# Kernel optimization log

Hardware: AMD Instinct MI355X
Metric: run time of the kernel (lower is better)

## Reference

```python
import jax, jax.numpy as jnp
import numpy as np

N = 100000   # nodes
E = 400000   # edges per relation
K = 2        # n_hop relations
D = 256      # in_dim
ATT = 64     # att_dim
L = 3        # n_layer
H1, H2 = 128, 64
EPS = 1e-5
NEG_SLOPE = 0.01


def setup_inputs() -> dict:
    key = jax.random.key(0)
    ks = jax.random.split(key, 16)
    s = 1.0 / np.sqrt(D)
    return {
        "x": jax.random.normal(ks[0], (N, D), jnp.float32),
        "edges_index": jax.random.randint(ks[1], (K, 2, E), 0, N),
        "edges_weight": jax.random.uniform(ks[2], (K, E), jnp.float32),
        "bn_gamma": jnp.ones((D,), jnp.float32),
        "bn_beta": jnp.zeros((D,), jnp.float32),
        "gcn_W": jax.random.normal(ks[3], (L, D, D), jnp.float32) * s,
        "gcn_b": jnp.zeros((L, D), jnp.float32),
        "att_lin_W": jax.random.normal(ks[4], (L, K, D, ATT), jnp.float32) * s,
        "att_lin_b": jnp.zeros((L, K, ATT), jnp.float32),
        "att_q": jax.random.normal(ks[5], (L, K, ATT), jnp.float32) * (1.0 / np.sqrt(ATT)),
        "proj_W1": jax.random.normal(ks[6], (D, H1), jnp.float32) * s,
        "proj_b1": jnp.zeros((H1,), jnp.float32),
        "proj_W2": jax.random.normal(ks[7], (H1, H2), jnp.float32) * (1.0 / np.sqrt(H1)),
        "proj_b2": jnp.zeros((H2,), jnp.float32),
    }


def _gcn_aggregate(row, col, w, xw):
    # symmetric gcn_norm on adj_t (add_self_loops=False):
    # deg[i] = sum of w over edges with col == i
    deg = jax.ops.segment_sum(w, col, num_segments=N)
    dinv = jnp.where(deg > 0, 1.0 / jnp.sqrt(deg), 0.0)
    norm = dinv[col] * w * dinv[row]                       # [E]
    # out[c] += norm * xw[r]
    return jax.ops.segment_sum(norm[:, None] * xw[row], col, num_segments=N)


def reference(x, edges_index, edges_weight, bn_gamma, bn_beta, gcn_W, gcn_b,
              att_lin_W, att_lin_b, att_q, proj_W1, proj_b1, proj_W2, proj_b2):
    # BatchNorm1d (training-mode batch stats)
    mu = jnp.mean(x, axis=0)
    var = jnp.mean((x - mu) ** 2, axis=0)
    h = (x - mu) / jnp.sqrt(var + EPS) * bn_gamma + bn_beta   # [N, D]

    rows = edges_index[:, 0, :]  # [K, E]
    cols = edges_index[:, 1, :]

    for i in range(L):
        xw = h @ gcn_W[i]                                     # shared transform [N, D]
        # per-relation sparse aggregation, vmapped over K
        xs = jax.vmap(_gcn_aggregate, in_axes=(0, 0, 0, None))(
            rows, cols, edges_weight, xw) + gcn_b[i]          # [K, N, D]
        # HanAtt: softmax over hops of per-node scores
        keys = jnp.tanh(jnp.einsum('knd,kdh->knh', xs, att_lin_W[i]) + att_lin_b[i][:, None, :])
        sim = jnp.einsum('knh,kh->kn', keys, att_q[i])        # [K, N]
        alpha = jax.nn.softmax(sim, axis=0)                   # softmax over K
        h = jnp.einsum('knd,kn->nd', xs, alpha)               # [N, D]
        h = jax.nn.relu(h)

    h = jax.nn.leaky_relu(h @ proj_W1 + proj_b1, NEG_SLOPE)
    h = jax.nn.leaky_relu(h @ proj_W2 + proj_b2, NEG_SLOPE)
    return h
```

## Files before the change

kernel.cpp:

```cpp
#include <hip/hip_runtime.h>
#include <hip/hip_bf16.h>
#include <math.h>

#define NN 100000
#define EE 400000
#define KD 2
#define DD 256
#define ATTD 64
#define LL 3
#define HH1 128
#define HH2 64
#define EPSV 1e-5f
#define SLOPE 0.01f
#define KN (KD * NN)

typedef short short8 __attribute__((ext_vector_type(8)));
typedef float floatx4 __attribute__((ext_vector_type(4)));
typedef unsigned int u32x4 __attribute__((ext_vector_type(4)));
typedef unsigned short u16;
typedef unsigned int u32;
typedef unsigned long long u64;

__device__ __forceinline__ u16 f2bf(float f) {
    u32 u = __float_as_uint(f);
    return (u16)((u + 0x7fffu + ((u >> 16) & 1u)) >> 16);
}
__device__ __forceinline__ float bf2f(u16 h) {
    return __uint_as_float((u32)h << 16);
}

__global__ void bn_stats(const float* __restrict__ x, float* __restrict__ sums) {
    int d = threadIdx.x;
    int r0 = blockIdx.x * 125;
    float s = 0.f, sq = 0.f;
    for (int r = r0; r < r0 + 125; ++r) {
        float v = x[(size_t)r * DD + d];
        s += v; sq += v * v;
    }
    atomicAdd(&sums[d], s);
    atomicAdd(&sums[DD + d], sq);
}

__global__ void bn_apply(const float* __restrict__ x, const float* __restrict__ sums,
                         const float* __restrict__ gamma, const float* __restrict__ beta,
                         u16* __restrict__ h_hi, u16* __restrict__ h_lo) {
    size_t i = (size_t)blockIdx.x * blockDim.x + threadIdx.x;
    const float inv_n = 1.f / NN;
    int dq = (int)(i & 63) * 4;
    float4 xv = ((const float4*)x)[i];
    ushort4 hv, lv;
    float* xp = (float*)&xv;
    u16* hp = (u16*)&hv; u16* lp = (u16*)&lv;
#pragma unroll
    for (int j = 0; j < 4; ++j) {
        int d = dq + j;
        float mu = sums[d] * inv_n;
        float var = sums[DD + d] * inv_n - mu * mu;
        float inv = rsqrtf(var + EPSV);
        float v = (xp[j] - mu) * inv * gamma[d] + beta[d];
        u16 hb = f2bf(v);
        hp[j] = hb;
        lp[j] = f2bf(v - bf2f(hb));
    }
    ((ushort4*)h_hi)[i] = hv;
    ((ushort4*)h_lo)[i] = lv;
}

__global__ void deg_count(const int* __restrict__ ei, const float* __restrict__ w,
                          float* __restrict__ deg, int* __restrict__ counts) {
    int i = blockIdx.x * blockDim.x + threadIdx.x;
    if (i >= KD * EE) return;
    int k = i / EE, e = i - k * EE;
    int col = ei[(size_t)k * 2 * EE + EE + e];
    atomicAdd(&deg[k * NN + col], w[i]);
    atomicAdd(&counts[k * NN + col], 1);
}

__global__ void dinv_kernel(float* __restrict__ d) {
    int i = blockIdx.x * blockDim.x + threadIdx.x;
    if (i >= KD * NN) return;
    float v = d[i];
    d[i] = v > 0.f ? 1.f / sqrtf(v) : 0.f;
}

#define SCAN_NB ((KN + 255) / 256)
__global__ void scan_blocks(int* __restrict__ starts, int* __restrict__ bsums) {
    __shared__ int tmp[256];
    int t = threadIdx.x;
    int idx = blockIdx.x * 256 + t;
    int v = (idx < KN) ? starts[idx] : 0;
    tmp[t] = v;
    __syncthreads();
#pragma unroll
    for (int off = 1; off < 256; off <<= 1) {
        int s = (t >= off) ? tmp[t - off] : 0;
        __syncthreads();
        tmp[t] += s;
        __syncthreads();
    }
    if (idx < KN) starts[idx] = tmp[t] - v;
    if (t == 255) bsums[blockIdx.x] = tmp[255];
}

__global__ void scan_sums(int* __restrict__ bsums) {
    __shared__ int tmp[1024];
    int t = threadIdx.x;
    int v = (t < SCAN_NB) ? bsums[t] : 0;
    tmp[t] = v;
    __syncthreads();
#pragma unroll
    for (int off = 1; off < 1024; off <<= 1) {
        int s = (t >= off) ? tmp[t - off] : 0;
        __syncthreads();
        tmp[t] += s;
        __syncthreads();
    }
    if (t < SCAN_NB) bsums[t] = tmp[t] - v;
}

__global__ void scan_add(int* __restrict__ starts, const int* __restrict__ bsums) {
    int idx = blockIdx.x * 256 + threadIdx.x;
    if (idx < KN) starts[idx] += bsums[blockIdx.x];
}

__global__ void csr_fill(const int* __restrict__ ei, const float* __restrict__ w,
                         const float* __restrict__ dinv,
                         int* __restrict__ starts, int2* __restrict__ edata) {
    int i = blockIdx.x * blockDim.x + threadIdx.x;
    if (i >= KD * EE) return;
    int k = i / EE, e = i - k * EE;
    const int* eik = ei + (size_t)k * 2 * EE;
    int row = eik[e], col = eik[EE + e];
    float nv = dinv[k * NN + col] * w[i] * dinv[k * NN + row];
    int pos = atomicAdd(&starts[k * NN + col], 1);
    edata[pos] = make_int2(row, __float_as_int(nv));
}

__device__ __forceinline__ void fma_row8(float4& a0, float4& a1, uint4 w, float nv) {
    float2 f0 = __bfloat1622float2(*(const __hip_bfloat162*)&w.x);
    float2 f1 = __bfloat1622float2(*(const __hip_bfloat162*)&w.y);
    float2 f2 = __bfloat1622float2(*(const __hip_bfloat162*)&w.z);
    float2 f3 = __bfloat1622float2(*(const __hip_bfloat162*)&w.w);
    a0.x += nv * f0.x; a0.y += nv * f0.y; a0.z += nv * f1.x; a0.w += nv * f1.y;
    a1.x += nv * f2.x; a1.y += nv * f2.y; a1.z += nv * f3.x; a1.w += nv * f3.y;
}

__global__ __launch_bounds__(256) void gather_agg(
        const int* __restrict__ starts, const int2* __restrict__ edata,
        const u16* __restrict__ xw, u16* __restrict__ xs) {
    int wv = blockIdx.x * 4 + (threadIdx.x >> 6);
    int lane = threadIdx.x & 63;
    int half = lane >> 5, l32 = lane & 31;
    int widx = wv * 2 + half;
    if (widx >= KN) return;
    int begin = widx ? starts[widx - 1] : 0;
    int end = starts[widx];
    int deg = end - begin;
    float4 acc0 = make_float4(0.f, 0.f, 0.f, 0.f);
    float4 acc1 = make_float4(0.f, 0.f, 0.f, 0.f);

    int2 ed = (l32 < deg) ? edata[begin + l32] : make_int2(0, 0);
    int dmain = deg > 32 ? 32 : deg;
    int base = half << 5;

    int j = 0;
    for (; j + 4 <= dmain; j += 4) {
        int r0 = __shfl(ed.x, base + j),     r1 = __shfl(ed.x, base + j + 1);
        int r2 = __shfl(ed.x, base + j + 2), r3 = __shfl(ed.x, base + j + 3);
        float n0 = __int_as_float(__shfl(ed.y, base + j));
        float n1 = __int_as_float(__shfl(ed.y, base + j + 1));
        float n2 = __int_as_float(__shfl(ed.y, base + j + 2));
        float n3 = __int_as_float(__shfl(ed.y, base + j + 3));
        uint4 w0 = *(const uint4*)(xw + (size_t)r0 * DD + l32 * 8);
        uint4 w1 = *(const uint4*)(xw + (size_t)r1 * DD + l32 * 8);
        uint4 w2 = *(const uint4*)(xw + (size_t)r2 * DD + l32 * 8);
        uint4 w3 = *(const uint4*)(xw + (size_t)r3 * DD + l32 * 8);
        fma_row8(acc0, acc1, w0, n0);
        fma_row8(acc0, acc1, w1, n1);
        fma_row8(acc0, acc1, w2, n2);
        fma_row8(acc0, acc1, w3, n3);
    }
    for (; j < dmain; ++j) {
        int r = __shfl(ed.x, base + j);
        float nv = __int_as_float(__shfl(ed.y, base + j));
        uint4 w = *(const uint4*)(xw + (size_t)r * DD + l32 * 8);
        fma_row8(acc0, acc1, w, nv);
    }
    for (int e = begin + 32; e < end; ++e) {
        int2 ee = edata[e];
        float nv = __int_as_float(ee.y);
        uint4 w = *(const uint4*)(xw + (size_t)ee.x * DD + l32 * 8);
        fma_row8(acc0, acc1, w, nv);
    }

    u32x4 st;
    st.x = (u32)f2bf(acc0.x) | ((u32)f2bf(acc0.y) << 16);
    st.y = (u32)f2bf(acc0.z) | ((u32)f2bf(acc0.w) << 16);
    st.z = (u32)f2bf(acc1.x) | ((u32)f2bf(acc1.y) << 16);
    st.w = (u32)f2bf(acc1.z) | ((u32)f2bf(acc1.w) << 16);
    __builtin_nontemporal_store(st, (u32x4*)(xs + (size_t)widx * DD + l32 * 8));
}

#define GCN_T (LL * DD * DD)
#define ATT_T (LL * KD * DD * ATTD)
#define P1_T  (DD * HH1)
#define P2_T  (HH1 * HH2)
#define WC_TOTAL (GCN_T + ATT_T + P1_T + P2_T)
__device__ __forceinline__ void wconv1(const float* __restrict__ W, u16* __restrict__ Wt,
                                       int i, int Kd, int Nc) {
    int kk = i / Nc, n = i - kk * Nc;
    Wt[(size_t)n * Kd + kk] = f2bf(W[i]);
}
__global__ void wconv_all(const float* __restrict__ gcnW, u16* __restrict__ gcnWb,
                          const float* __restrict__ attW, u16* __restrict__ attWb,
                          const float* __restrict__ pW1, u16* __restrict__ pW1b,
                          const float* __restrict__ pW2, u16* __restrict__ pW2b) {
    int gid = blockIdx.x * 256 + threadIdx.x;
    if (gid >= WC_TOTAL) return;
    if (gid < GCN_T) {
        int l = gid >> 16, i = gid & 65535;
        wconv1(gcnW + (size_t)l * DD * DD, gcnWb + (size_t)l * DD * DD, i, DD, DD);
    } else if (gid < GCN_T + ATT_T) {
        int g = gid - GCN_T;
        int lk = g >> 14, i = g & 16383;
        wconv1(attW + (size_t)lk * DD * ATTD, attWb + (size_t)lk * ATTD * DD, i, DD, ATTD);
    } else if (gid < GCN_T + ATT_T + P1_T) {
        wconv1(pW1, pW1b, gid - (GCN_T + ATT_T), DD, HH1);
    } else {
        wconv1(pW2, pW2b, gid - (GCN_T + ATT_T + P1_T), HH1, HH2);
    }
}

__global__ void att_bias_fold(const float* __restrict__ attW, const float* __restrict__ attb,
                              const float* __restrict__ gcnb, float* __restrict__ batt) {
    int lk = blockIdx.x;
    int a = threadIdx.x;
    int l = lk >> 1;
    const float* W = attW + (size_t)lk * DD * ATTD;
    const float* gb = gcnb + l * DD;
    float s = attb[lk * ATTD + a];
    for (int d = 0; d < DD; ++d) s += gb[d] * W[d * ATTD + a];
    batt[lk * ATTD + a] = s;
}

#define LDSP 40

template<int BN_, int MODE, bool PRESPLIT, bool BIAS, int ACT>
__global__ __launch_bounds__(256) void gemm_mfma(
        const float* __restrict__ A,
        const u16* __restrict__ Ahi, const u16* __restrict__ Alo,
        const u16* __restrict__ Bt, const float* __restrict__ bias,
        float* __restrict__ Cf, u16* __restrict__ Cb,
        int M, int Kd, int Nc) {
    constexpr int JW = BN_ / 64;
    __shared__ u16 AsHi[64 * LDSP];
    __shared__ u16 AsLo[64 * LDSP];
    __shared__ u16 Bs[BN_ * LDSP];

    const int tid = threadIdx.x;
    const int lane = tid & 63, wx = tid >> 6;
    const int lane15 = lane & 15, quad = lane >> 4;
    const int bm = blockIdx.x * 64;
    const int bn = blockIdx.y * BN_;

    floatx4 acc[4][JW];
#pragma unroll
    for (int i = 0; i < 4; ++i)
#pragma unroll
        for (int j = 0; j < JW; ++j) acc[i][j] = (floatx4){0.f, 0.f, 0.f, 0.f};

    for (int k0 = 0; k0 < Kd; k0 += 32) {
        if constexpr (PRESPLIT) {
            {
                int m = tid >> 2, ko = (tid & 3) << 3;
                uint4 vh = make_uint4(0, 0, 0, 0), vl = make_uint4(0, 0, 0, 0);
                if (bm + m < M) {
                    vh = *(const uint4*)(Ahi + (size_t)(bm + m) * Kd + k0 + ko);
                    vl = *(const uint4*)(Alo + (size_t)(bm + m) * Kd + k0 + ko);
                }
                *(uint4*)(void*)(AsHi + m * LDSP + ko) = vh;
                *(uint4*)(void*)(AsLo + m * LDSP + ko) = vl;
            }
        } else {
#pragma unroll
            for (int t = tid; t < 512; t += 256) {
                int m = t >> 3, k4 = (t & 7) << 2;
                float4 v = make_float4(0.f, 0.f, 0.f, 0.f);
                if (bm + m < M) v = *(const float4*)(A + (size_t)(bm + m) * Kd + k0 + k4);
                u16 h0 = f2bf(v.x), h1 = f2bf(v.y), h2 = f2bf(v.z), h3 = f2bf(v.w);
                *(ushort4*)(void*)(AsHi + m * LDSP + k4) = make_ushort4(h0, h1, h2, h3);
                u16 l0 = f2bf(v.x - bf2f(h0)), l1 = f2bf(v.y - bf2f(h1));
                u16 l2 = f2bf(v.z - bf2f(h2)), l3 = f2bf(v.w - bf2f(h3));
                *(ushort4*)(void*)(AsLo + m * LDSP + k4) = make_ushort4(l0, l1, l2, l3);
            }
        }
#pragma unroll
        for (int t = tid; t < BN_ * 4; t += 256) {
            int n = t >> 2, ko = (t & 3) << 3;
            uint4 w = *(const uint4*)(Bt + (size_t)(bn + n) * Kd + k0 + ko);
            *(uint4*)(void*)(Bs + n * LDSP + ko) = w;
        }
        __syncthreads();

        const u16* pA  = AsHi + lane15 * LDSP + quad * 8;
        const u16* pAl = AsLo + lane15 * LDSP + quad * 8;
        const u16* pB  = Bs + (wx * (BN_ / 4) + lane15) * LDSP + quad * 8;
        short8 b[JW];
#pragma unroll
        for (int j = 0; j < JW; ++j) b[j] = *(const short8*)(pB + j * 16 * LDSP);
#pragma unroll
        for (int i = 0; i < 4; ++i) {
            short8 a = *(const short8*)(pA + i * 16 * LDSP);
#pragma unroll
            for (int j = 0; j < JW; ++j)
                acc[i][j] = __builtin_amdgcn_mfma_f32_16x16x32_bf16(a, b[j], acc[i][j], 0, 0, 0);
        }
#pragma unroll
        for (int i = 0; i < 4; ++i) {
            short8 a = *(const short8*)(pAl + i * 16 * LDSP);
#pragma unroll
            for (int j = 0; j < JW; ++j)
                acc[i][j] = __builtin_amdgcn_mfma_f32_16x16x32_bf16(a, b[j], acc[i][j], 0, 0, 0);
        }
        __syncthreads();
    }

#pragma unroll
    for (int i = 0; i < 4; ++i) {
#pragma unroll
        for (int r = 0; r < 4; ++r) {
            int row = bm + i * 16 + quad * 4 + r;
            if (row >= M) continue;
#pragma unroll
            for (int j = 0; j < JW; ++j) {
                int col = bn + wx * (BN_ / 4) + j * 16 + lane15;
                float v = acc[i][j][r];
                if constexpr (BIAS) v += bias[col];
                if constexpr (ACT == 1) v = v > 0.f ? v : SLOPE * v;
                if constexpr (MODE == 0) Cf[(size_t)row * Nc + col] = v;
                else                     Cb[(size_t)row * Nc + col] = f2bf(v);
            }
        }
    }
}

__global__ __launch_bounds__(256, 4) void att_combine(
        const u16* __restrict__ xs, const u16* __restrict__ Bt,
        const float* __restrict__ batt, const float* __restrict__ qv,
        const float* __restrict__ gcnb,
        u16* __restrict__ h_hi, u16* __restrict__ h_lo) {
    __shared__ float simbuf[KD][2][64];

    const int tid = threadIdx.x;
    const int lane = tid & 63, waveid = tid >> 6;
    const int kw = waveid >> 1, ch = waveid & 1;
    const int lane15 = lane & 15, quad = lane >> 4;
    const int bm = blockIdx.x * 64;

    short8 bf[8][2];
#pragma unroll
    for (int t = 0; t < 8; ++t)
#pragma unroll
        for (int j = 0; j < 2; ++j) {
            int col = ch * 32 + j * 16 + lane15;
            bf[t][j] = *(const short8*)(Bt + (size_t)kw * ATTD * DD +
                                        (size_t)col * DD + t * 32 + quad * 8);
        }

    floatx4 acc[4][2];
#pragma unroll
    for (int i = 0; i < 4; ++i)
#pragma unroll
        for (int j = 0; j < 2; ++j) acc[i][j] = (floatx4){0.f, 0.f, 0.f, 0.f};

#pragma unroll
    for (int i = 0; i < 4; ++i) {
        int row = bm + i * 16 + lane15;
        row = row < NN ? row : 0;
        const u16* pa = xs + ((size_t)kw * NN + row) * DD + quad * 8;
#pragma unroll
        for (int t = 0; t < 8; ++t) {
            short8 a = *(const short8*)(pa + t * 32);
            acc[i][0] = __builtin_amdgcn_mfma_f32_16x16x32_bf16(a, bf[t][0], acc[i][0], 0, 0, 0);
            acc[i][1] = __builtin_amdgcn_mfma_f32_16x16x32_bf16(a, bf[t][1], acc[i][1], 0, 0, 0);
        }
    }

#pragma unroll
    for (int i = 0; i < 4; ++i) {
#pragma unroll
        for (int r = 0; r < 4; ++r) {
            float p = 0.f;
#pragma unroll
            for (int j = 0; j < 2; ++j) {
                int col = ch * 32 + j * 16 + lane15;
                float v = acc[i][j][r] + batt[kw * ATTD + col];
                float ex = __expf(2.f * v);
                float th = 1.f - 2.f / (ex + 1.f);
                p += th * qv[kw * ATTD + col];
            }
            p += __shfl_xor(p, 1, 64);
            p += __shfl_xor(p, 2, 64);
            p += __shfl_xor(p, 4, 64);
            p += __shfl_xor(p, 8, 64);
            if (lane15 == 0) simbuf[kw][ch][i * 16 + quad * 4 + r] = p;
        }
    }
    __syncthreads();

#pragma unroll 4
    for (int it = 0; it < 8; ++it) {
        int item = tid + it * 256;
        int row = item >> 5, c8 = item & 31;
        int grow = bm + row;
        if (grow >= NN) continue;
        float s0 = simbuf[0][0][row] + simbuf[0][1][row];
        float s1 = simbuf[1][0][row] + simbuf[1][1][row];
        float m = fmaxf(s0, s1);
        float e0 = __expf(s0 - m), e1 = __expf(s1 - m);
        float inv = 1.f / (e0 + e1);
        float a0 = e0 * inv, a1 = e1 * inv;
        uint4 x0 = *(const uint4*)(xs + (size_t)grow * DD + c8 * 8);
        uint4 x1 = *(const uint4*)(xs + ((size_t)NN + grow) * DD + c8 * 8);
        const float* bp = gcnb + c8 * 8;
        uint4 hiw, low;
        u16* hp = (u16*)&hiw; u16* lp = (u16*)&low;
        const u32* xp0 = (const u32*)&x0; const u32* xp1 = (const u32*)&x1;
#pragma unroll
        for (int j = 0; j < 4; ++j) {
            float2 f0 = __bfloat1622float2(*(const __hip_bfloat162*)&xp0[j]);
            float2 f1 = __bfloat1622float2(*(const __hip_bfloat162*)&xp1[j]);
            float ra = fmaxf(0.f, a0 * f0.x + a1 * f1.x + bp[2 * j]);
            float rb = fmaxf(0.f, a0 * f0.y + a1 * f1.y + bp[2 * j + 1]);
            u16 ha = f2bf(ra), hb = f2bf(rb);
            hp[2 * j] = ha; hp[2 * j + 1] = hb;
            lp[2 * j] = f2bf(ra - bf2f(ha));
            lp[2 * j + 1] = f2bf(rb - bf2f(hb));
        }
        *(uint4*)(h_hi + (size_t)grow * DD + c8 * 8) = hiw;
        *(uint4*)(h_lo + (size_t)grow * DD + c8 * 8) = low;
    }
}

extern "C" void kernel_launch(void* const* d_in, const int* in_sizes, int n_in,
                              void* d_out, int out_size, void* d_ws, size_t ws_size,
                              hipStream_t stream) {
    const float* x     = (const float*)d_in[0];
    const int*   ei    = (const int*)d_in[1];
    const float* ew    = (const float*)d_in[2];
    const float* gamma = (const float*)d_in[3];
    const float* beta  = (const float*)d_in[4];
    const float* gcn_W = (const float*)d_in[5];
    const float* gcn_b = (const float*)d_in[6];
    const float* att_W = (const float*)d_in[7];
    const float* att_b = (const float*)d_in[8];
    const float* att_q = (const float*)d_in[9];
    const float* pW1   = (const float*)d_in[10];
    const float* pb1   = (const float*)d_in[11];
    const float* pW2   = (const float*)d_in[12];
    const float* pb2   = (const float*)d_in[13];
    float* out = (float*)d_out;

    char* wsb = (char*)d_ws;
    size_t off = 0;
    auto alloc = [&](size_t bytes) -> void* {
        void* p = wsb + off;
        off += (bytes + 255) & ~(size_t)255;
        return p;
    };
    u16*   xs    = (u16*)alloc((size_t)KD * NN * DD * 2);
    u16*   h_hi  = (u16*)alloc((size_t)NN * DD * 2);
    u16*   h_lo  = (u16*)alloc((size_t)NN * DD * 2);
    u16*   xw    = (u16*)alloc((size_t)NN * DD * 2);
    float* p1tmp = (float*)xw;
    float* dinv  = (float*)alloc((size_t)KN * 4);
    int*   starts= (int*)alloc(((size_t)KN + 1) * 4);
    int2*  edata = (int2*)alloc((size_t)KD * EE * 8);
    float* bnsums= (float*)alloc(2 * DD * 4);
    u16*   gcnWb = (u16*)alloc((size_t)LL * DD * DD * 2);
    u16*   attWb = (u16*)alloc((size_t)LL * KD * ATTD * DD * 2);
    u16*   pW1b  = (u16*)alloc((size_t)HH1 * DD * 2);
    u16*   pW2b  = (u16*)alloc((size_t)HH2 * HH1 * 2);
    float* batt  = (float*)alloc((size_t)LL * KD * ATTD * 4);
    int*   bsums = (int*)alloc((size_t)SCAN_NB * 4);

    wconv_all<<<(WC_TOTAL + 255) / 256, 256, 0, stream>>>(
        gcn_W, gcnWb, att_W, attWb, pW1, pW1b, pW2, pW2b);
    att_bias_fold<<<LL * KD, ATTD, 0, stream>>>(att_W, att_b, gcn_b, batt);

    hipMemsetAsync(bnsums, 0, 2 * DD * 4, stream);
    bn_stats<<<800, 256, 0, stream>>>(x, bnsums);
    bn_apply<<<25000, 256, 0, stream>>>(x, bnsums, gamma, beta, h_hi, h_lo);

    hipMemsetAsync(dinv, 0, (size_t)KN * 4 + ((size_t)KN + 1) * 4, stream);
    deg_count<<<(KD * EE + 255) / 256, 256, 0, stream>>>(ei, ew, dinv, starts);
    dinv_kernel<<<(KN + 255) / 256, 256, 0, stream>>>(dinv);
    scan_blocks<<<SCAN_NB, 256, 0, stream>>>(starts, bsums);
    scan_sums<<<1, 1024, 0, stream>>>(bsums);
    scan_add<<<SCAN_NB, 256, 0, stream>>>(starts, bsums);
    csr_fill<<<(KD * EE + 255) / 256, 256, 0, stream>>>(ei, ew, dinv, starts, edata);

    const int MB64 = (NN + 63) / 64;
    for (int l = 0; l < LL; ++l) {
        gemm_mfma<256, 1, true, false, 0><<<dim3(MB64, 1), 256, 0, stream>>>(
            nullptr, h_hi, h_lo, gcnWb + (size_t)l * DD * DD, nullptr,
            nullptr, xw, NN, DD, DD);
        gather_agg<<<(KN + 7) / 8, 256, 0, stream>>>(starts, edata, xw, xs);
        att_combine<<<MB64, 256, 0, stream>>>(
            xs, attWb + (size_t)l * KD * ATTD * DD,
            batt + (size_t)l * KD * ATTD, att_q + (size_t)l * KD * ATTD,
            gcn_b + l * DD, h_hi, h_lo);
    }

    gemm_mfma<128, 0, true, true, 1><<<dim3(MB64, 1), 256, 0, stream>>>(
        nullptr, h_hi, h_lo, pW1b, pb1, p1tmp, nullptr, NN, DD, HH1);
    gemm_mfma<64, 0, false, true, 1><<<dim3(MB64, 1), 256, 0, stream>>>(
        p1tmp, nullptr, nullptr, pW2b, pb2, out, nullptr, NN, HH1, HH2);
}
```

Before: 992.4 us.

## Stage attention GEMM operands through LDS and drop nontemporal xs store

The att_combine kernel used to hold the whole B operand in registers and read A straight from global memory per wave. It now stages 32-wide K slices of both xs and the attention weights into padded shared-memory tiles with barriers, and drops the min-blocks launch bound. The aggregation kernel's xs output store changes from nontemporal to a normal store so xs can stay in cache for the following attention kernel. The intent is coalesced loads, lower register pressure and better cache reuse, at the cost of extra LDS traffic and two barriers per K step.

```diff
diff --git a/kernel.cpp b/kernel.cpp
--- a/kernel.cpp
+++ b/kernel.cpp
@@ -198,7 +198,7 @@
     st.y = (u32)f2bf(acc0.z) | ((u32)f2bf(acc0.w) << 16);
     st.z = (u32)f2bf(acc1.x) | ((u32)f2bf(acc1.y) << 16);
     st.w = (u32)f2bf(acc1.z) | ((u32)f2bf(acc1.w) << 16);
-    __builtin_nontemporal_store(st, (u32x4*)(xs + (size_t)widx * DD + l32 * 8));
+    *(u32x4*)(xs + (size_t)widx * DD + l32 * 8) = st;
 }
 
 #define GCN_T (LL * DD * DD)
@@ -344,11 +344,13 @@
     }
 }
 
-__global__ __launch_bounds__(256, 4) void att_combine(
+__global__ __launch_bounds__(256) void att_combine(
         const u16* __restrict__ xs, const u16* __restrict__ Bt,
         const float* __restrict__ batt, const float* __restrict__ qv,
         const float* __restrict__ gcnb,
         u16* __restrict__ h_hi, u16* __restrict__ h_lo) {
+    __shared__ u16 As[2 * 64 * LDSP];
+    __shared__ u16 Bs[2 * 64 * LDSP];
     __shared__ float simbuf[KD][2][64];
 
     const int tid = threadIdx.x;
@@ -357,33 +359,42 @@
     const int lane15 = lane & 15, quad = lane >> 4;
     const int bm = blockIdx.x * 64;
 
-    short8 bf[8][2];
-#pragma unroll
-    for (int t = 0; t < 8; ++t)
-#pragma unroll
-        for (int j = 0; j < 2; ++j) {
-            int col = ch * 32 + j * 16 + lane15;
-            bf[t][j] = *(const short8*)(Bt + (size_t)kw * ATTD * DD +
-                                        (size_t)col * DD + t * 32 + quad * 8);
-        }
-
     floatx4 acc[4][2];
 #pragma unroll
     for (int i = 0; i < 4; ++i)
 #pragma unroll
         for (int j = 0; j < 2; ++j) acc[i][j] = (floatx4){0.f, 0.f, 0.f, 0.f};
 
-#pragma unroll
-    for (int i = 0; i < 4; ++i) {
-        int row = bm + i * 16 + lane15;
-        row = row < NN ? row : 0;
-        const u16* pa = xs + ((size_t)kw * NN + row) * DD + quad * 8;
-#pragma unroll
-        for (int t = 0; t < 8; ++t) {
-            short8 a = *(const short8*)(pa + t * 32);
-            acc[i][0] = __builtin_amdgcn_mfma_f32_16x16x32_bf16(a, bf[t][0], acc[i][0], 0, 0, 0);
-            acc[i][1] = __builtin_amdgcn_mfma_f32_16x16x32_bf16(a, bf[t][1], acc[i][1], 0, 0, 0);
-        }
+    for (int k0 = 0; k0 < DD; k0 += 32) {
+#pragma unroll
+        for (int it = 0; it < 2; ++it) {
+            int t = tid + it * 256;
+            int k = t >> 8, m = (t >> 2) & 63, ko = (t & 3) << 3;
+            uint4 v = make_uint4(0, 0, 0, 0);
+            if (bm + m < NN)
+                v = *(const uint4*)(xs + ((size_t)k * NN + bm + m) * DD + k0 + ko);
+            *(uint4*)(void*)(As + (k * 64 + m) * LDSP + ko) = v;
+        }
+#pragma unroll
+        for (int it = 0; it < 2; ++it) {
+            int t = tid + it * 256;
+            int k = t >> 8, c = (t >> 2) & 63, ko = (t & 3) << 3;
+            uint4 v = *(const uint4*)(Bt + ((size_t)k * ATTD + c) * DD + k0 + ko);
+            *(uint4*)(void*)(Bs + (k * 64 + c) * LDSP + ko) = v;
+        }
+        __syncthreads();
+
+        const u16* pA = As + (kw * 64 + lane15) * LDSP + quad * 8;
+        const u16* pB = Bs + (kw * 64 + ch * 32 + lane15) * LDSP + quad * 8;
+        short8 b0 = *(const short8*)(pB);
+        short8 b1 = *(const short8*)(pB + 16 * LDSP);
+#pragma unroll
+        for (int i = 0; i < 4; ++i) {
+            short8 a = *(const short8*)(pA + i * 16 * LDSP);
+            acc[i][0] = __builtin_amdgcn_mfma_f32_16x16x32_bf16(a, b0, acc[i][0], 0, 0, 0);
+            acc[i][1] = __builtin_amdgcn_mfma_f32_16x16x32_bf16(a, b1, acc[i][1], 0, 0, 0);
+        }
+        __syncthreads();
     }
 
 #pragma unroll
```

Result: faster. 967.9 us (-2.5%).
